# Performance work log

Measured on AMD Instinct MI355X. Metric: run time of the kernel, lower is better.

## Reference

```python
import jax, jax.numpy as jnp
import numpy as np

B, H, W, DIM, WS, SHIFT, HEADS = 32, 56, 56, 256, 7, 3, 8
N = WS * WS          # 49 tokens per window
C2 = 2 * DIM         # concatenated two-modal channel dim
NW = (H // WS) * (W // WS)


def _rel_index(ws):
    coords = np.stack(np.meshgrid(np.arange(ws), np.arange(ws), indexing='ij')).reshape(2, -1)
    rel = (coords[:, :, None] - coords[:, None, :]).transpose(1, 2, 0)
    rel[:, :, 0] += ws - 1
    rel[:, :, 1] += ws - 1
    rel[:, :, 0] *= 2 * ws - 1
    return rel.sum(-1)  # (N, N) int

REL_IDX = _rel_index(WS).reshape(-1)


def _attn_mask():
    # standard Swin shifted-window mask: 0 / -100 per window pair
    img = np.zeros((H, W))
    cnt = 0
    for hs in (slice(0, H - WS), slice(H - WS, H - SHIFT), slice(H - SHIFT, H)):
        for ws_ in (slice(0, W - WS), slice(W - WS, W - SHIFT), slice(W - SHIFT, W)):
            img[hs, ws_] = cnt
            cnt += 1
    mw = img.reshape(H // WS, WS, W // WS, WS).transpose(0, 2, 1, 3).reshape(-1, N)
    d = mw[:, None, :] - mw[:, :, None]
    return np.where(d != 0, -100.0, 0.0).astype(np.float32)  # (nW, N, N)

ATTN_MASK = _attn_mask()


def _win_part(x):  # (B,H,W,C) -> (nW*B, N, C)
    b, c = x.shape[0], x.shape[-1]
    x = x.reshape(b, H // WS, WS, W // WS, WS, c).transpose(0, 1, 3, 2, 4, 5)
    return x.reshape(-1, N, c)


def _win_rev(w, b):  # (nW*B, N, C) -> (B,H,W,C)
    c = w.shape[-1]
    x = w.reshape(b, H // WS, W // WS, WS, WS, c).transpose(0, 1, 3, 2, 4, 5)
    return x.reshape(b, H, W, c)


def _ln(t, g, bb):
    m = t.mean(-1, keepdims=True)
    v = t.var(-1, keepdims=True)
    return (t - m) / jnp.sqrt(v + 1e-5) * g + bb


def setup_inputs() -> dict:
    key = jax.random.key(0)
    ks = jax.random.split(key, 8)
    def nrm(k, shape, s=0.02):
        return jax.random.normal(k, shape, jnp.float32) * s
    return {
        'x': jax.random.normal(ks[0], (B, H * W, DIM), jnp.float32),
        'y': jax.random.normal(ks[1], (B, H * W, DIM), jnp.float32),
        'g1': jnp.ones((DIM,), jnp.float32), 'b1': jnp.zeros((DIM,), jnp.float32),
        'rpb': nrm(ks[2], ((2 * WS - 1) * (2 * WS - 1), HEADS)),
        'w_qkv': nrm(ks[3], (6 * DIM, 2 * DIM)), 'b_qkv': jnp.zeros((6 * DIM,), jnp.float32),
        'w_proj': nrm(ks[4], (DIM, 2 * DIM)), 'b_proj': jnp.zeros((DIM,), jnp.float32),
        'g2': jnp.ones((DIM,), jnp.float32), 'b2': jnp.zeros((DIM,), jnp.float32),
        'w_fc1': nrm(ks[5], (4 * DIM, DIM)), 'b_fc1': jnp.zeros((4 * DIM,), jnp.float32),
        'w_fc2': nrm(ks[6], (DIM, 4 * DIM)), 'b_fc2': jnp.zeros((DIM,), jnp.float32),
    }


def reference(x, y, g1, b1, rpb, w_qkv, b_qkv, w_proj, b_proj, g2, b2, w_fc1, b_fc1, w_fc2, b_fc2):
    scale = (DIM // HEADS) ** -0.5  # as in __init__: head_dim = dim // num_heads
    shortcut = x
    xn = _ln(x, g1, b1).reshape(B, H, W, DIM)
    yn = _ln(y, g1, b1).reshape(B, H, W, DIM)
    # cyclic shift
    xn = jnp.roll(xn, (-SHIFT, -SHIFT), axis=(1, 2))
    yn = jnp.roll(yn, (-SHIFT, -SHIFT), axis=(1, 2))
    xw, yw = _win_part(xn), _win_part(yn)            # (nW*B, N, C)
    xy = jnp.concatenate([xw, yw], axis=-1)          # (nW*B, N, 2C)
    nwb, hd = xy.shape[0], C2 // HEADS
    qkv = (xy @ w_qkv.T + b_qkv).reshape(nwb, N, 3, HEADS, hd).transpose(2, 0, 3, 1, 4)
    q, k, v = qkv[0] * scale, qkv[1], qkv[2]         # (nW*B, h, N, d)
    attn = jnp.einsum('whnd,whmd->whnm', q, k)
    bias = rpb[REL_IDX].reshape(N, N, HEADS).transpose(2, 0, 1)  # (h, N, N)
    attn = attn + bias[None]
    attn = attn.reshape(B, NW, HEADS, N, N) + jnp.asarray(ATTN_MASK)[None, :, None]
    attn = jax.nn.softmax(attn.reshape(nwb, HEADS, N, N), axis=-1)
    out = jnp.einsum('whnm,whmd->whnd', attn, v).transpose(0, 2, 1, 3).reshape(nwb, N, C2)
    out = out @ w_proj.T + b_proj                    # fuse 2C -> C
    out = _win_rev(out, B)
    out = jnp.roll(out, (SHIFT, SHIFT), axis=(1, 2)).reshape(B, H * W, DIM)
    x = shortcut + out
    h = _ln(x, g2, b2)
    h = jax.nn.gelu(h @ w_fc1.T + b_fc1, approximate=False)
    return x + h @ w_fc2.T + b_fc2
```

## Files before the change

kernel.cpp:

```cpp
#include <hip/hip_runtime.h>
#include <hip/hip_bf16.h>

#define DEVI __device__ __forceinline__

typedef __attribute__((ext_vector_type(8))) short short8;
typedef __attribute__((ext_vector_type(4))) float f32x4;
typedef unsigned int u32;
typedef unsigned short u16;

typedef __attribute__((address_space(1))) const u32 gu32_t;
typedef __attribute__((address_space(3))) u32 lu32_t;

DEVI u16 f2bf(float f) {
  u32 u = __builtin_bit_cast(u32, f);
  u32 r = (u + 0x7fffu + ((u >> 16) & 1u)) >> 16;
  return (u16)r;
}

DEVI f32x4 mfma16(short8 a, short8 b, f32x4 c) {
  return __builtin_amdgcn_mfma_f32_16x16x32_bf16(a, b, c, 0, 0, 0);
}

DEVI void gload16(const void* g, void* l) {
  __builtin_amdgcn_global_load_lds((gu32_t*)g, (lu32_t*)l, 16, 0, 0);
}

DEVI float gelu_t(float v) {
  const float u = v * (0.7978845608f + 0.0356774081f * v * v);
  const float t = 1.0f - 2.0f / (__expf(2.0f * u) + 1.0f);
  return 0.5f * v * (1.0f + t);
}

#define CHUNK_ROWS 25088
#define PLANE ((size_t)CHUNK_ROWS * 64)
#define KOFF  ((size_t)8 * PLANE)
#define VOFF  ((size_t)16 * PLANE)

__global__ __launch_bounds__(256) void convk(const float* __restrict__ s, u16* __restrict__ d, int n4) {
  int i = blockIdx.x * 256 + threadIdx.x;
  if (i < n4) {
    const float4 v = ((const float4*)s)[i];
    ushort4 o;
    o.x = f2bf(v.x); o.y = f2bf(v.y); o.z = f2bf(v.z); o.w = f2bf(v.w);
    ((ushort4*)d)[i] = o;
  }
}

__global__ __launch_bounds__(256) void btab_build(const float* __restrict__ rpb, float* __restrict__ btab) {
  const int cls = blockIdx.x >> 3, h = blockIdx.x & 7;
  float* dst = btab + (size_t)(cls * 8 + h) * 4096;
  for (int e = threadIdx.x; e < 4096; e += 256) {
    const int n = e >> 6, m = e & 63;
    float v;
    if (m >= 49) {
      v = -1e30f;
    } else if (n >= 49) {
      v = 0.f;
    } else {
      const int r1 = n / 7, c1 = n - r1 * 7;
      const int r2 = m / 7, c2 = m - r2 * 7;
      const int rel = (r1 - r2 + 6) * 13 + (c1 - c2 + 6);
      v = rpb[rel * 8 + h];
      const int reg1 = ((cls & 1) ? (r1 < 4 ? 1 : 2) : 0) * 3 + ((cls & 2) ? (c1 < 4 ? 1 : 2) : 0);
      const int reg2 = ((cls & 1) ? (r2 < 4 ? 1 : 2) : 0) * 3 + ((cls & 2) ? (c2 < 4 ? 1 : 2) : 0);
      if (reg1 != reg2) v -= 100.f;
    }
    dst[e] = v;
  }
}

__global__ __launch_bounds__(256) void ln_gather(
    const float* __restrict__ x, const float* __restrict__ y,
    const float* __restrict__ g1, const float* __restrict__ b1,
    u16* __restrict__ XY, int rowbase)
{
  const int wv = threadIdx.x >> 6, lane = threadIdx.x & 63;
  const int rl = blockIdx.x * 4 + wv;
  const int row = rowbase + rl;
  const int w = row / 49, n = row - w * 49;
  const int b = w >> 6, win = w & 63, wh = win >> 3, ww = win & 7;
  const int r = n / 7, c = n - r * 7;
  int oh = wh * 7 + r + 3; if (oh >= 56) oh -= 56;
  int ow = ww * 7 + c + 3; if (ow >= 56) ow -= 56;
  const size_t po = ((size_t)b * 3136 + oh * 56 + ow) * 256;
  const float4 g1v = ((const float4*)g1)[lane];
  const float4 b1v = ((const float4*)b1)[lane];
  u16* orow = XY + (size_t)rl * 512;
  #pragma unroll
  for (int mod = 0; mod < 2; ++mod) {
    const float* src = (mod ? y : x) + po;
    const float4 v = ((const float4*)src)[lane];
    float s = v.x + v.y + v.z + v.w;
    #pragma unroll
    for (int off = 1; off < 64; off <<= 1) s += __shfl_xor(s, off);
    const float mean = s * (1.0f / 256.0f);
    const float d0 = v.x - mean, d1 = v.y - mean, d2 = v.z - mean, d3 = v.w - mean;
    float sq = d0 * d0 + d1 * d1 + d2 * d2 + d3 * d3;
    #pragma unroll
    for (int off = 1; off < 64; off <<= 1) sq += __shfl_xor(sq, off);
    const float rstd = rsqrtf(sq * (1.0f / 256.0f) + 1e-5f);
    ushort4 o;
    o.x = f2bf(d0 * rstd * g1v.x + b1v.x);
    o.y = f2bf(d1 * rstd * g1v.y + b1v.y);
    o.z = f2bf(d2 * rstd * g1v.z + b1v.z);
    o.w = f2bf(d3 * rstd * g1v.w + b1v.w);
    *(ushort4*)(orow + mod * 256 + lane * 4) = o;
  }
}

__global__ __launch_bounds__(256) void qkv_gemm(
    const u16* __restrict__ A, const u16* __restrict__ Bw,
    const float* __restrict__ bias, u16* __restrict__ Qo)
{
  __shared__ __align__(16) u16 smem[128 * 128];
  u16* sA = smem;
  u16* sB = smem + 128 * 64;
  const int nx = gridDim.x;
  const int nwg = nx * gridDim.y;
  const int orig = blockIdx.y * nx + blockIdx.x;
  const int sw = (orig & 7) * (nwg >> 3) + (orig >> 3);
  const int m0  = (sw / nx) * 128;
  const int nn0 = (sw % nx) * 128;
  const int tid = threadIdx.x;
  const int lane = tid & 63;
  const int wv = tid >> 6;
  const int wm = wv >> 1, wn = wv & 1;
  const int rq = lane & 15, kg = lane >> 4;
  f32x4 acc[4][4];
  #pragma unroll
  for (int i = 0; i < 4; ++i)
    #pragma unroll
    for (int j = 0; j < 4; ++j) acc[i][j] = f32x4{0,0,0,0};

  for (int kt = 0; kt < 8; ++kt) {
    if (kt) __syncthreads();
    #pragma unroll
    for (int i = 0; i < 4; ++i) {
      const int c = i * 256 + tid;
      gload16(A + (size_t)(m0 + (c >> 3)) * 512 + kt * 64 + (c & 7) * 8, sA + c * 8);
    }
    #pragma unroll
    for (int i = 0; i < 4; ++i) {
      const int c = i * 256 + tid;
      gload16(Bw + (size_t)(nn0 + (c >> 3)) * 512 + kt * 64 + (c & 7) * 8, sB + c * 8);
    }
    __syncthreads();
    #pragma unroll
    for (int k0 = 0; k0 < 2; ++k0) {
      short8 af[4], bf8[4];
      #pragma unroll
      for (int mt = 0; mt < 4; ++mt)
        af[mt] = *(const short8*)(sA + (wm * 64 + mt * 16 + rq) * 64 + k0 * 32 + kg * 8);
      #pragma unroll
      for (int nt = 0; nt < 4; ++nt)
        bf8[nt] = *(const short8*)(sB + (wn * 64 + nt * 16 + rq) * 64 + k0 * 32 + kg * 8);
      #pragma unroll
      for (int mt = 0; mt < 4; ++mt)
        #pragma unroll
        for (int nt = 0; nt < 4; ++nt)
          acc[mt][nt] = mfma16(af[mt], bf8[nt], acc[mt][nt]);
    }
  }
  __syncthreads();
  const int t = nn0 >> 9;
  const int hbase = (nn0 & 511) >> 6;
  const float sc = (t == 0) ? 0.17677669529663687f : 1.0f;
  #pragma unroll
  for (int nt = 0; nt < 4; ++nt) {
    const int col = wn * 64 + nt * 16 + rq;
    const float bc = bias[nn0 + col];
    const int c = col >> 3;
    #pragma unroll
    for (int mt = 0; mt < 4; ++mt)
      #pragma unroll
      for (int r = 0; r < 4; ++r) {
        const int row = wm * 64 + mt * 16 + kg * 4 + r;
        smem[row * 128 + (((c & 8) | ((c ^ row) & 7)) << 3) + (col & 7)] =
            f2bf((acc[mt][nt][r] + bc) * sc);
      }
  }
  __syncthreads();
  #pragma unroll
  for (int it = 0; it < 8; ++it) {
    const int cc = it * 256 + tid;
    const int row = cc >> 4, c = cc & 15;
    const int col = c * 8;
    const int hh = col >> 6, d = col & 63;
    const short8 v = *(const short8*)(smem + row * 128 + (((c & 8) | ((c ^ row) & 7)) << 3));
    *(short8*)(Qo + (size_t)(t * 8 + hbase + hh) * PLANE + (size_t)(m0 + row) * 64 + d) = v;
  }
}

__global__ __launch_bounds__(256, 3) void attn3(
    const u16* __restrict__ qkv, const float* __restrict__ btab,
    u16* __restrict__ concat, int wbase)
{
  __shared__ __align__(16) u16 sP[4][3136];
  __shared__ __align__(16) u16 sVT[4][4608];

  const int tid = threadIdx.x;
  const int wv = tid >> 6, lane = tid & 63;
  const int rq = lane & 15, kg = lane >> 4;
  const int gw = blockIdx.x * 4 + wv;
  const int wl = gw >> 3, h = gw & 7;
  const int w = wbase + wl;
  const int win = w & 63, wh = win >> 3, ww = win & 7;
  const int cls = ((wh == 7) ? 1 : 0) | ((ww == 7) ? 2 : 0);
  const float* Tb = btab + (size_t)(cls * 8 + h) * 4096;
  u16* sPw = sP[wv];
  u16* sVw = sVT[wv];

  const u16* qbase = qkv + (size_t)h * PLANE + (size_t)wl * 49 * 64;
  const u16* kbase = qkv + KOFF + (size_t)h * PLANE + (size_t)wl * 49 * 64;
  const u16* vbase = qkv + VOFF + (size_t)h * PLANE + (size_t)wl * 49 * 64;

  short8 vreg[4][2];
  #pragma unroll
  for (int t = 0; t < 4; ++t)
    #pragma unroll
    for (int h2 = 0; h2 < 2; ++h2)
      vreg[t][h2] = *(const short8*)(vbase + (size_t)(16 * t + rq) * 64 + kg * 8 + h2 * 32);

  short8 ak[4][2];
  #pragma unroll
  for (int j = 0; j < 4; ++j) {
    const int rr = (16 * j + rq) > 48 ? 48 : (16 * j + rq);
    ak[j][0] = *(const short8*)(kbase + rr * 64 + kg * 8);
    ak[j][1] = *(const short8*)(kbase + rr * 64 + 32 + kg * 8);
  }
  f32x4 sacc[4][4];
  #pragma unroll
  for (int i = 0; i < 4; ++i)
    #pragma unroll
    for (int j = 0; j < 4; ++j) sacc[i][j] = f32x4{0,0,0,0};
  #pragma unroll
  for (int i = 0; i < 4; ++i) {
    const int rr = (16 * i + rq) > 48 ? 48 : (16 * i + rq);
    const short8 a0 = *(const short8*)(qbase + rr * 64 + kg * 8);
    const short8 a1 = *(const short8*)(qbase + rr * 64 + 32 + kg * 8);
    #pragma unroll
    for (int j = 0; j < 4; ++j) {
      sacc[i][j] = mfma16(a0, ak[j][0], sacc[i][j]);
      sacc[i][j] = mfma16(a1, ak[j][1], sacc[i][j]);
    }
  }

  #pragma unroll
  for (int t = 0; t < 4; ++t) {
    const int row = 16 * t + rq;
    #pragma unroll
    for (int h2 = 0; h2 < 2; ++h2) {
      const int c0 = kg * 8 + h2 * 32;
      #pragma unroll
      for (int j = 0; j < 8; ++j)
        sVw[(c0 + j) * 72 + (row ^ (kg << 4))] = (u16)vreg[t][h2][j];
    }
  }

  #pragma unroll
  for (int i = 0; i < 4; ++i) {
    #pragma unroll
    for (int r = 0; r < 4; ++r) {
      const int n = 16 * i + kg * 4 + r;
      const float* Trow = Tb + n * 64 + rq;
      float pv[4];
      #pragma unroll
      for (int j = 0; j < 4; ++j)
        pv[j] = sacc[i][j][r] + Trow[16 * j];
      float mx = fmaxf(fmaxf(pv[0], pv[1]), fmaxf(pv[2], pv[3]));
      #pragma unroll
      for (int off = 1; off < 16; off <<= 1) mx = fmaxf(mx, __shfl_xor(mx, off));
      float sm = 0.f;
      #pragma unroll
      for (int j = 0; j < 4; ++j) { const float e = __expf(pv[j] - mx); pv[j] = e; sm += e; }
      #pragma unroll
      for (int off = 1; off < 16; off <<= 1) sm += __shfl_xor(sm, off);
      const float inv = 1.0f / sm;
      if (n < 49) {
        #pragma unroll
        for (int j = 0; j < 4; ++j) {
          const int col = 16 * j + rq;
          sPw[n * 64 + (((col >> 3) ^ (n & 7)) << 3) + (col & 7)] = f2bf(pv[j] * inv);
        }
      }
    }
  }

  f32x4 oacc[4][4];
  #pragma unroll
  for (int i = 0; i < 4; ++i)
    #pragma unroll
    for (int j = 0; j < 4; ++j) oacc[i][j] = f32x4{0,0,0,0};
  #pragma unroll
  for (int m0v = 0; m0v < 2; ++m0v) {
    short8 av[4];
    #pragma unroll
    for (int ct = 0; ct < 4; ++ct) {
      const int col = ct * 16 + rq;
      const int s = (col >> 3) & 3;
      short8 vvv = *(const short8*)(sVw + col * 72 + ((m0v * 32 + kg * 8) ^ (s << 4)));
      if (m0v == 1) {
        if (kg == 3) {
          #pragma unroll
          for (int e = 0; e < 8; ++e) vvv[e] = 0;
        } else if (kg == 2) {
          #pragma unroll
          for (int e = 1; e < 8; ++e) vvv[e] = 0;
        }
      }
      av[ct] = vvv;
    }
    #pragma unroll
    for (int i = 0; i < 4; ++i) {
      const int rr = (16 * i + rq) > 48 ? 48 : (16 * i + rq);
      const int ch = (m0v * 4 + kg) ^ (rr & 7);
      const short8 pa = *(const short8*)(sPw + rr * 64 + ch * 8);
      #pragma unroll
      for (int ct = 0; ct < 4; ++ct)
        oacc[i][ct] = mfma16(pa, av[ct], oacc[i][ct]);
    }
  }

  __builtin_amdgcn_s_waitcnt(0);
  #pragma unroll
  for (int i = 0; i < 4; ++i)
    #pragma unroll
    for (int ct = 0; ct < 4; ++ct)
      #pragma unroll
      for (int r = 0; r < 4; ++r) {
        const int n = 16 * i + kg * 4 + r;
        if (n < 49) {
          const int col = ct * 16 + rq;
          sPw[n * 64 + (((col >> 3) ^ (n & 7)) << 3) + (col & 7)] = f2bf(oacc[i][ct][r]);
        }
      }
  u16* crow = concat + (size_t)(wl * 49) * 512 + h * 64;
  #pragma unroll
  for (int it = 0; it < 7; ++it) {
    const int c = it * 64 + lane;
    if (c < 392) {
      const int m = c >> 3, s = c & 7;
      const short8 vvv = *(const short8*)(sPw + m * 64 + ((s ^ (m & 7)) << 3));
      *(short8*)(crow + (size_t)m * 512 + s * 8) = vvv;
    }
  }
}

__global__ __launch_bounds__(256, 2) void projln(
    const u16* __restrict__ A, const u16* __restrict__ Bw,
    const float* __restrict__ bias, const float* __restrict__ x,
    const float* __restrict__ g2, const float* __restrict__ b2,
    float* __restrict__ out, u16* __restrict__ xn2, int rowbase)
{
  __shared__ __align__(16) u16 sA[128 * 64];
  __shared__ __align__(16) u16 sB[256 * 64];
  const int m0 = blockIdx.x * 128;
  const int tid = threadIdx.x;
  const int lane = tid & 63;
  const int wv = tid >> 6;
  const int rq = lane & 15, kg = lane >> 4;
  f32x4 acc[2][16];
  #pragma unroll
  for (int i = 0; i < 2; ++i)
    #pragma unroll
    for (int j = 0; j < 16; ++j) acc[i][j] = f32x4{0,0,0,0};

  for (int kt = 0; kt < 8; ++kt) {
    if (kt) __syncthreads();
    #pragma unroll
    for (int i = 0; i < 4; ++i) {
      const int c = i * 256 + tid;
      gload16(A + (size_t)(m0 + (c >> 3)) * 512 + kt * 64 + (c & 7) * 8, sA + c * 8);
    }
    #pragma unroll
    for (int i = 0; i < 8; ++i) {
      const int c = i * 256 + tid;
      gload16(Bw + (size_t)(c >> 3) * 512 + kt * 64 + (c & 7) * 8, sB + c * 8);
    }
    __syncthreads();
    #pragma unroll
    for (int k0 = 0; k0 < 2; ++k0) {
      short8 af[2];
      #pragma unroll
      for (int mt = 0; mt < 2; ++mt)
        af[mt] = *(const short8*)(sA + (wv * 32 + mt * 16 + rq) * 64 + k0 * 32 + kg * 8);
      #pragma unroll
      for (int nt = 0; nt < 16; ++nt) {
        const short8 bf8 = *(const short8*)(sB + (nt * 16 + rq) * 64 + k0 * 32 + kg * 8);
        #pragma unroll
        for (int mt = 0; mt < 2; ++mt)
          acc[mt][nt] = mfma16(af[mt], bf8, acc[mt][nt]);
      }
    }
  }

  float br[16], g2r[16], b2r[16];
  #pragma unroll
  for (int nt = 0; nt < 16; ++nt) {
    const int col = nt * 16 + rq;
    br[nt] = bias[col]; g2r[nt] = g2[col]; b2r[nt] = b2[col];
  }
  #pragma unroll
  for (int mt = 0; mt < 2; ++mt) {
    #pragma unroll
    for (int r = 0; r < 4; ++r) {
      const int row = m0 + wv * 32 + mt * 16 + kg * 4 + r;
      const u32 g = (u32)(rowbase + row);
      const u32 w = g / 49u; const u32 n = g - w * 49u;
      const int b = w >> 6, win = w & 63, wh = win >> 3, ww = win & 7;
      const u32 rr = n / 7u; const u32 cc = n - rr * 7u;
      int oh = wh * 7 + (int)rr + 3; if (oh >= 56) oh -= 56;
      int ow = ww * 7 + (int)cc + 3; if (ow >= 56) ow -= 56;
      const size_t po = ((size_t)b * 3136 + oh * 56 + ow) * 256;
      float vals[16];
      float s = 0.f;
      #pragma unroll
      for (int nt = 0; nt < 16; ++nt) {
        const float v = acc[mt][nt][r] + br[nt] + x[po + nt * 16 + rq];
        vals[nt] = v; s += v;
      }
      #pragma unroll
      for (int off = 1; off < 16; off <<= 1) s += __shfl_xor(s, off);
      const float mean = s * (1.0f / 256.0f);
      float sq = 0.f;
      #pragma unroll
      for (int nt = 0; nt < 16; ++nt) { const float d_ = vals[nt] - mean; sq += d_ * d_; }
      #pragma unroll
      for (int off = 1; off < 16; off <<= 1) sq += __shfl_xor(sq, off);
      const float rstd = rsqrtf(sq * (1.0f / 256.0f) + 1e-5f);
      #pragma unroll
      for (int nt = 0; nt < 16; ++nt) {
        const int col = nt * 16 + rq;
        out[po + col] = vals[nt];
        xn2[po + col] = f2bf((vals[nt] - mean) * rstd * g2r[nt] + b2r[nt]);
      }
    }
  }
}

__global__ __launch_bounds__(256, 2) void fused_mlp(
    const u16* __restrict__ xn2, const u16* __restrict__ w1,
    const float* __restrict__ bf1, const u16* __restrict__ w2,
    const float* __restrict__ bf2v, float* __restrict__ out)
{
  __shared__ __align__(16) u16 sX[64 * 256];
  __shared__ __align__(16) u16 sH[64 * 256];

  const int m0 = blockIdx.x * 64;
  const int tid = threadIdx.x;
  const int wv = tid >> 6, lane = tid & 63;
  const int rq = lane & 15, kg = lane >> 4;

  #pragma unroll
  for (int i = 0; i < 8; ++i) {
    const int c = i * 256 + tid;
    const int row = c >> 5, ch = c & 31;
    const int sch = (ch & 24) | ((ch ^ row) & 7);
    gload16(xn2 + (size_t)(m0 + row) * 256 + sch * 8, sX + c * 8);
  }

  f32x4 acc2[4][4];
  #pragma unroll
  for (int i = 0; i < 4; ++i)
    #pragma unroll
    for (int j = 0; j < 4; ++j) acc2[i][j] = f32x4{0,0,0,0};

  __syncthreads();

  for (int t = 0; t < 4; ++t) {
    f32x4 a1[4][4];
    #pragma unroll
    for (int i = 0; i < 4; ++i)
      #pragma unroll
      for (int j = 0; j < 4; ++j) a1[i][j] = f32x4{0,0,0,0};
    #pragma unroll
    for (int ks = 0; ks < 8; ++ks) {
      short8 bfr[4];
      #pragma unroll
      for (int nt = 0; nt < 4; ++nt)
        bfr[nt] = *(const short8*)(w1 + (size_t)(t * 256 + wv * 64 + nt * 16 + rq) * 256 + ks * 32 + kg * 8);
      #pragma unroll
      for (int mt = 0; mt < 4; ++mt) {
        const int R = mt * 16 + rq;
        const int wk = ks * 4 + kg;
        const short8 af = *(const short8*)(sX + R * 256 + ((wk & 24) | ((wk ^ R) & 7)) * 8);
        #pragma unroll
        for (int nt = 0; nt < 4; ++nt)
          a1[mt][nt] = mfma16(af, bfr[nt], a1[mt][nt]);
      }
    }
    __syncthreads();
    #pragma unroll
    for (int nt = 0; nt < 4; ++nt) {
      const int col = wv * 64 + nt * 16 + rq;
      const float bb = bf1[t * 256 + col];
      const int c = col >> 3;
      #pragma unroll
      for (int mt = 0; mt < 4; ++mt)
        #pragma unroll
        for (int r = 0; r < 4; ++r) {
          const int row = mt * 16 + kg * 4 + r;
          sH[row * 256 + ((c & 24) | ((c ^ row) & 7)) * 8 + (col & 7)] =
              f2bf(gelu_t(a1[mt][nt][r] + bb));
        }
    }
    __syncthreads();
    #pragma unroll
    for (int ks = 0; ks < 8; ++ks) {
      short8 bfr2[4];
      #pragma unroll
      for (int nt = 0; nt < 4; ++nt)
        bfr2[nt] = *(const short8*)(w2 + (size_t)(wv * 64 + nt * 16 + rq) * 1024 + t * 256 + ks * 32 + kg * 8);
      #pragma unroll
      for (int mt = 0; mt < 4; ++mt) {
        const int R = mt * 16 + rq;
        const int wk = ks * 4 + kg;
        const short8 af = *(const short8*)(sH + R * 256 + ((wk & 24) | ((wk ^ R) & 7)) * 8);
        #pragma unroll
        for (int nt = 0; nt < 4; ++nt)
          acc2[mt][nt] = mfma16(af, bfr2[nt], acc2[mt][nt]);
      }
    }
  }

  #pragma unroll
  for (int nt = 0; nt < 4; ++nt) {
    const int col = wv * 64 + nt * 16 + rq;
    const float bb = bf2v[col];
    #pragma unroll
    for (int mt = 0; mt < 4; ++mt)
      #pragma unroll
      for (int r = 0; r < 4; ++r) {
        float* p = out + (size_t)(m0 + mt * 16 + kg * 4 + r) * 256 + col;
        *p = acc2[mt][nt][r] + bb + *p;
      }
  }
}

extern "C" void kernel_launch(void* const* d_in, const int* in_sizes, int n_in,
                              void* d_out, int out_size, void* d_ws, size_t ws_size,
                              hipStream_t stream) {
  const float* x      = (const float*)d_in[0];
  const float* y      = (const float*)d_in[1];
  const float* g1     = (const float*)d_in[2];
  const float* b1     = (const float*)d_in[3];
  const float* rpb    = (const float*)d_in[4];
  const float* w_qkv  = (const float*)d_in[5];
  const float* b_qkv  = (const float*)d_in[6];
  const float* w_proj = (const float*)d_in[7];
  const float* b_proj = (const float*)d_in[8];
  const float* g2     = (const float*)d_in[9];
  const float* b2     = (const float*)d_in[10];
  const float* w_fc1  = (const float*)d_in[11];
  const float* b_fc1  = (const float*)d_in[12];
  const float* w_fc2  = (const float*)d_in[13];
  const float* b_fc2  = (const float*)d_in[14];
  float* out = (float*)d_out;

  u16* wsp = (u16*)d_ws;
  u16* wqkv_bf  = wsp;
  u16* wproj_bf = wsp + 786432;
  u16* wfc1_bf  = wsp + 917504;
  u16* wfc2_bf  = wsp + 1179648;
  float* btab   = (float*)(wsp + 1441792);
  u16* xn2      = wsp + 1703936;
  u16* XYc      = wsp + 27394048;
  u16* qkvc     = wsp + 40239104;

  convk<<<768, 256, 0, stream>>>(w_qkv,  wqkv_bf,  196608);
  convk<<<128, 256, 0, stream>>>(w_proj, wproj_bf, 32768);
  convk<<<256, 256, 0, stream>>>(w_fc1,  wfc1_bf,  65536);
  convk<<<256, 256, 0, stream>>>(w_fc2,  wfc2_bf,  65536);
  btab_build<<<32, 256, 0, stream>>>(rpb, btab);

  for (int c = 0; c < 4; ++c) {
    ln_gather<<<6272, 256, 0, stream>>>(x, y, g1, b1, XYc, c * CHUNK_ROWS);
    qkv_gemm<<<dim3(12, 196), 256, 0, stream>>>(XYc, wqkv_bf, b_qkv, qkvc);
    attn3<<<1024, 256, 0, stream>>>(qkvc, btab, XYc, c * 512);
    projln<<<196, 256, 0, stream>>>(XYc, wproj_bf, b_proj, x, g2, b2, out, xn2, c * CHUNK_ROWS);
  }

  fused_mlp<<<1568, 256, 0, stream>>>(xn2, wfc1_bf, b_fc1, wfc2_bf, b_fc2, out);
}
```

Measured before the change: 854.1 us.

## Shrink MLP hidden chunk to 128, prefetch weight fragments, raise occupancy

The fused MLP kernel now processes the 1024-wide hidden dimension in eight chunks of 128 instead of four of 256. This halves the sH shared buffer so three blocks can fit per CU (launch bounds raised to 3). W1 fragments are software-pipelined three k-steps ahead, and W2 fragments are loaded before the barriers so global latency overlaps the GELU store and the MFMAs. The trade-offs are more loop iterations and barriers, and tighter register pressure under the higher occupancy bound, which could cause spills.

```diff
diff --git a/kernel.cpp b/kernel.cpp
--- a/kernel.cpp
+++ b/kernel.cpp
@@ -438,13 +438,13 @@
   }
 }
 
-__global__ __launch_bounds__(256, 2) void fused_mlp(
+__global__ __launch_bounds__(256, 3) void fused_mlp(
     const u16* __restrict__ xn2, const u16* __restrict__ w1,
     const float* __restrict__ bf1, const u16* __restrict__ w2,
     const float* __restrict__ bf2v, float* __restrict__ out)
 {
   __shared__ __align__(16) u16 sX[64 * 256];
-  __shared__ __align__(16) u16 sH[64 * 256];
+  __shared__ __align__(16) u16 sH[64 * 128];
 
   const int m0 = blockIdx.x * 64;
   const int tid = threadIdx.x;
@@ -467,58 +467,85 @@
 
   __syncthreads();
 
-  for (int t = 0; t < 4; ++t) {
-    f32x4 a1[4][4];
+  for (int t = 0; t < 8; ++t) {
+    short8 w1f[4][2];
+    #pragma unroll
+    for (int p = 0; p < 3; ++p)
+      #pragma unroll
+      for (int nt = 0; nt < 2; ++nt)
+        w1f[p][nt] = *(const short8*)(w1 + (size_t)(t * 128 + wv * 32 + nt * 16 + rq) * 256 + p * 32 + kg * 8);
+    f32x4 a1[4][2];
     #pragma unroll
     for (int i = 0; i < 4; ++i)
       #pragma unroll
-      for (int j = 0; j < 4; ++j) a1[i][j] = f32x4{0,0,0,0};
+      for (int j = 0; j < 2; ++j) a1[i][j] = f32x4{0,0,0,0};
     #pragma unroll
     for (int ks = 0; ks < 8; ++ks) {
-      short8 bfr[4];
-      #pragma unroll
-      for (int nt = 0; nt < 4; ++nt)
-        bfr[nt] = *(const short8*)(w1 + (size_t)(t * 256 + wv * 64 + nt * 16 + rq) * 256 + ks * 32 + kg * 8);
+      if (ks < 5) {
+        #pragma unroll
+        for (int nt = 0; nt < 2; ++nt)
+          w1f[(ks + 3) & 3][nt] = *(const short8*)(w1 + (size_t)(t * 128 + wv * 32 + nt * 16 + rq) * 256 + (ks + 3) * 32 + kg * 8);
+      }
       #pragma unroll
       for (int mt = 0; mt < 4; ++mt) {
         const int R = mt * 16 + rq;
         const int wk = ks * 4 + kg;
         const short8 af = *(const short8*)(sX + R * 256 + ((wk & 24) | ((wk ^ R) & 7)) * 8);
         #pragma unroll
-        for (int nt = 0; nt < 4; ++nt)
-          a1[mt][nt] = mfma16(af, bfr[nt], a1[mt][nt]);
+        for (int nt = 0; nt < 2; ++nt)
+          a1[mt][nt] = mfma16(af, w1f[ks & 3][nt], a1[mt][nt]);
       }
     }
     __syncthreads();
-    #pragma unroll
-    for (int nt = 0; nt < 4; ++nt) {
-      const int col = wv * 64 + nt * 16 + rq;
-      const float bb = bf1[t * 256 + col];
-      const int c = col >> 3;
+    short8 w2f[2][4];
+    #pragma unroll
+    for (int p = 0; p < 2; ++p)
+      #pragma unroll
+      for (int nt = 0; nt < 4; ++nt)
+        w2f[p][nt] = *(const short8*)(w2 + (size_t)(wv * 64 + nt * 16 + rq) * 1024 + t * 128 + p * 32 + kg * 8);
+    #pragma unroll
+    for (int nt = 0; nt < 2; ++nt) {
+      const int col = wv * 32 + nt * 16 + rq;
+      const float bb = bf1[t * 128 + col];
+      const int ch = col >> 3;
       #pragma unroll
       for (int mt = 0; mt < 4; ++mt)
         #pragma unroll
         for (int r = 0; r < 4; ++r) {
           const int row = mt * 16 + kg * 4 + r;
-          sH[row * 256 + ((c & 24) | ((c ^ row) & 7)) * 8 + (col & 7)] =
+          sH[row * 128 + ((ch & 8) | ((ch ^ row) & 7)) * 8 + (col & 7)] =
               f2bf(gelu_t(a1[mt][nt][r] + bb));
         }
     }
     __syncthreads();
-    #pragma unroll
-    for (int ks = 0; ks < 8; ++ks) {
-      short8 bfr2[4];
+    short8 w2g[2][4];
+    #pragma unroll
+    for (int p = 0; p < 2; ++p)
       #pragma unroll
       for (int nt = 0; nt < 4; ++nt)
-        bfr2[nt] = *(const short8*)(w2 + (size_t)(wv * 64 + nt * 16 + rq) * 1024 + t * 256 + ks * 32 + kg * 8);
+        w2g[p][nt] = *(const short8*)(w2 + (size_t)(wv * 64 + nt * 16 + rq) * 1024 + t * 128 + (2 + p) * 32 + kg * 8);
+    #pragma unroll
+    for (int ks = 0; ks < 2; ++ks) {
       #pragma unroll
       for (int mt = 0; mt < 4; ++mt) {
         const int R = mt * 16 + rq;
         const int wk = ks * 4 + kg;
-        const short8 af = *(const short8*)(sH + R * 256 + ((wk & 24) | ((wk ^ R) & 7)) * 8);
+        const short8 af = *(const short8*)(sH + R * 128 + ((wk & 8) | ((wk ^ R) & 7)) * 8);
         #pragma unroll
         for (int nt = 0; nt < 4; ++nt)
-          acc2[mt][nt] = mfma16(af, bfr2[nt], acc2[mt][nt]);
+          acc2[mt][nt] = mfma16(af, w2f[ks][nt], acc2[mt][nt]);
+      }
+    }
+    #pragma unroll
+    for (int ks = 0; ks < 2; ++ks) {
+      #pragma unroll
+      for (int mt = 0; mt < 4; ++mt) {
+        const int R = mt * 16 + rq;
+        const int wk = (2 + ks) * 4 + kg;
+        const short8 af = *(const short8*)(sH + R * 128 + ((wk & 8) | ((wk ^ R) & 7)) * 8);
+        #pragma unroll
+        for (int nt = 0; nt < 4; ++nt)
+          acc2[mt][nt] = mfma16(af, w2g[ks][nt], acc2[mt][nt]);
       }
     }
   }
```

Measured after the change: 908.2 us. 6.3% more time.
